# Optimization experiments

Measured on AMD Instinct MI355X. Metric: run time of the kernel, lower is better.

## Reference

```python
import jax, jax.numpy as jnp
import numpy as np

K = 16  # number of neighbors (init kwarg k)


def setup_inputs() -> dict:
    key = jax.random.key(0)
    k1, k2 = jax.random.split(key)
    B, N, D, F = 2, 2048, 16, 64
    points = jax.random.normal(k1, (B, N, D), dtype=jnp.float32)
    features = jax.random.normal(k2, (B, N, F), dtype=jnp.float32)
    return {"features": features, "points": points}


def reference(features, points):
    # points: [B, N, D]
    B, N, _ = points.shape
    # Pairwise Euclidean distances via broadcasted subtraction, matching
    # tf.norm(points[:, :, None] - points[:, None, :], axis=-1): [B, N, N]
    diff = points[:, :, None, :] - points[:, None, :, :]
    distance = jnp.sqrt(jnp.sum(diff * diff, axis=-1))
    # top (k+1) smallest distances == top_k of negated distance; drop self (col 0)
    _, topk_indices = jax.lax.top_k(-distance, K + 1)  # [B, N, K+1] int32
    topk_indices = topk_indices[:, :, 1:]               # [B, N, K]
    batch_indices = jnp.broadcast_to(
        jnp.arange(B, dtype=jnp.int32)[:, None, None, None], (B, N, K, 1)
    )
    # [B, N, K, 2] -> (batch_idx, neighbor_idx) pairs for gather_nd-style use
    return jnp.concatenate([batch_indices, topk_indices[..., None]], axis=3)
```

## Files before the change

kernel.cpp:

```cpp
#include <hip/hip_runtime.h>
#include <stdint.h>


#define NPTS 2048
#define DIMS 16
#define KK 16
#define THREADS 256
#define PER_THREAD (NPTS / THREADS)
#define HPL (THREADS / 64)

__device__ __forceinline__ void ce(uint64_t& a, uint64_t& b) {
    uint64_t lo = (a < b) ? a : b;
    uint64_t hi = (a < b) ? b : a;
    a = lo; b = hi;
}

__global__ __launch_bounds__(THREADS) void knn_kernel(
    const float* __restrict__ points, int* __restrict__ out)
{
    const int q = blockIdx.x;
    const int b = q >> 11;
    const int n = q & (NPTS - 1);
    const float* bp = points + (size_t)b * NPTS * DIMS;

    __shared__ uint64_t skeys[PER_THREAD][THREADS];
    __shared__ float    qs[DIMS];

    const int tid = threadIdx.x;
    if (tid < DIMS) qs[tid] = bp[(size_t)n * DIMS + tid];
    __syncthreads();

    float qp[DIMS];
#pragma unroll
    for (int d = 0; d < DIMS; ++d) qp[d] = qs[d];

    uint64_t k[PER_THREAD];
#pragma unroll
    for (int i = 0; i < PER_THREAD; ++i) {
        const int c = tid + i * THREADS;
        const float4* cp4 = (const float4*)(bp + (size_t)c * DIMS);
        float s[DIMS];
#pragma unroll
        for (int v = 0; v < 4; ++v) {
            float4 cv = cp4[v];
            float d0 = qp[4 * v + 0] - cv.x;
            float d1 = qp[4 * v + 1] - cv.y;
            float d2_ = qp[4 * v + 2] - cv.z;
            float d3 = qp[4 * v + 3] - cv.w;
            s[4 * v + 0] = __fmul_rn(d0, d0);
            s[4 * v + 1] = __fmul_rn(d1, d1);
            s[4 * v + 2] = __fmul_rn(d2_, d2_);
            s[4 * v + 3] = __fmul_rn(d3, d3);
        }
        float r0 = __fadd_rn(s[0], s[8]);
        float r1 = __fadd_rn(s[1], s[9]);
        float r2 = __fadd_rn(s[2], s[10]);
        float r3 = __fadd_rn(s[3], s[11]);
        float r4 = __fadd_rn(s[4], s[12]);
        float r5 = __fadd_rn(s[5], s[13]);
        float r6 = __fadd_rn(s[6], s[14]);
        float r7 = __fadd_rn(s[7], s[15]);
        float t0 = __fadd_rn(r0, r1);
        float t1 = __fadd_rn(r2, r3);
        float t2 = __fadd_rn(r4, r5);
        float t3 = __fadd_rn(r6, r7);
        float d2 = __fadd_rn(__fadd_rn(t0, t1), __fadd_rn(t2, t3));
        float dist = __fsqrt_rn(d2);
        k[i] = ((uint64_t)__float_as_uint(dist) << 32) | (uint32_t)c;
    }

    ce(k[0], k[1]); ce(k[2], k[3]); ce(k[4], k[5]); ce(k[6], k[7]);
    ce(k[0], k[2]); ce(k[1], k[3]); ce(k[4], k[6]); ce(k[5], k[7]);
    ce(k[1], k[2]); ce(k[5], k[6]);
    ce(k[0], k[4]); ce(k[1], k[5]); ce(k[2], k[6]); ce(k[3], k[7]);
    ce(k[1], k[4]); ce(k[3], k[6]);
    ce(k[2], k[4]); ce(k[3], k[5]);
    ce(k[3], k[4]);

#pragma unroll
    for (int j = 0; j < PER_THREAD; ++j) skeys[j][tid] = k[j];
    __syncthreads();

    if (tid >= 64) return;
    const int lane = tid;

    uint64_t head[HPL];
    int      pos[HPL];
#pragma unroll
    for (int h = 0; h < HPL; ++h) {
        head[h] = skeys[0][lane + 64 * h];
        pos[h] = 1;
    }

    for (int r = 0; r <= KK; ++r) {
        uint64_t m = head[0]; int hm = 0;
#pragma unroll
        for (int h = 1; h < HPL; ++h)
            if (head[h] < m) { m = head[h]; hm = h; }
        uint64_t g = m;
#pragma unroll
        for (int off = 1; off < 64; off <<= 1) {
            uint64_t o = (uint64_t)__shfl_xor((unsigned long long)g, off, 64);
            if (o < g) g = o;
        }
        if (m == g) {
            if (r > 0) {
                const int idx = (int)(uint32_t)(g & 0xffffffffu);
                const size_t o = (((size_t)q * KK) + (size_t)(r - 1)) * 2;
                out[o]     = b;
                out[o + 1] = idx;
            }
#pragma unroll
            for (int h = 0; h < HPL; ++h) {
                if (hm == h) {
                    head[h] = (pos[h] < PER_THREAD) ? skeys[pos[h]][lane + 64 * h]
                                                    : ~0ull;
                    pos[h]++;
                }
            }
        }
    }
}

extern "C" void kernel_launch(void* const* d_in, const int* in_sizes, int n_in,
                              void* d_out, int out_size, void* d_ws, size_t ws_size,
                              hipStream_t stream) {
    (void)d_ws; (void)ws_size; (void)out_size;
    const float* points;
    if (n_in >= 2 && in_sizes[1] == 2 * 2048 * 16) {
        points = (const float*)d_in[1];
    } else if (n_in >= 1 && in_sizes[0] == 2 * 2048 * 16) {
        points = (const float*)d_in[0];
    } else {
        points = (const float*)d_in[n_in - 1];
    }
    int* out = (int*)d_out;
    knn_kernel<<<2 * 2048, THREADS, 0, stream>>>(points, out);
}
```

Measured before the change: 92.35 us.

## Process four queries per block and select top-k with one wave per query

```diff
diff --git a/kernel.cpp b/kernel.cpp
--- a/kernel.cpp
+++ b/kernel.cpp
@@ -6,8 +6,11 @@
 #define DIMS 16
 #define KK 16
 #define THREADS 256
-#define PER_THREAD (NPTS / THREADS)
-#define HPL (THREADS / 64)
+#define NQ 4
+#define CPT (NPTS / THREADS)
+#define PER_LANE (NPTS / 64)
+#define RUNS 4
+#define RLEN 8
 
 __device__ __forceinline__ void ce(uint64_t& a, uint64_t& b) {
     uint64_t lo = (a < b) ? a : b;
@@ -15,88 +18,94 @@
     a = lo; b = hi;
 }
 
-__global__ __launch_bounds__(THREADS) void knn_kernel(
+__global__ __launch_bounds__(THREADS, 4) void knn_kernel(
     const float* __restrict__ points, int* __restrict__ out)
 {
-    const int q = blockIdx.x;
-    const int b = q >> 11;
-    const int n = q & (NPTS - 1);
+    const int qbase = blockIdx.x * NQ;
+    const int b = qbase >> 11;
     const float* bp = points + (size_t)b * NPTS * DIMS;
 
-    __shared__ uint64_t skeys[PER_THREAD][THREADS];
-    __shared__ float    qs[DIMS];
+    __shared__ float dist[NQ][NPTS];
 
     const int tid = threadIdx.x;
-    if (tid < DIMS) qs[tid] = bp[(size_t)n * DIMS + tid];
+
+    float qp[NQ][DIMS];
+#pragma unroll
+    for (int w = 0; w < NQ; ++w) {
+        const int n = (qbase + w) & (NPTS - 1);
+        const float4* qp4 = (const float4*)(bp + (size_t)n * DIMS);
+#pragma unroll
+        for (int v = 0; v < 4; ++v) {
+            float4 t = qp4[v];
+            qp[w][4 * v + 0] = t.x; qp[w][4 * v + 1] = t.y;
+            qp[w][4 * v + 2] = t.z; qp[w][4 * v + 3] = t.w;
+        }
+    }
+
+#pragma unroll 2
+    for (int i = 0; i < CPT; ++i) {
+        const int c = tid + i * THREADS;
+        const float4* cp4 = (const float4*)(bp + (size_t)c * DIMS);
+        float cv[DIMS];
+#pragma unroll
+        for (int v = 0; v < 4; ++v) {
+            float4 t = cp4[v];
+            cv[4 * v + 0] = t.x; cv[4 * v + 1] = t.y;
+            cv[4 * v + 2] = t.z; cv[4 * v + 3] = t.w;
+        }
+#pragma unroll
+        for (int w = 0; w < NQ; ++w) {
+            float s[DIMS];
+#pragma unroll
+            for (int d = 0; d < DIMS; ++d) {
+                float df = qp[w][d] - cv[d];
+                s[d] = __fmul_rn(df, df);
+            }
+            float r0 = __fadd_rn(s[0], s[8]);
+            float r1 = __fadd_rn(s[1], s[9]);
+            float r2 = __fadd_rn(s[2], s[10]);
+            float r3 = __fadd_rn(s[3], s[11]);
+            float r4 = __fadd_rn(s[4], s[12]);
+            float r5 = __fadd_rn(s[5], s[13]);
+            float r6 = __fadd_rn(s[6], s[14]);
+            float r7 = __fadd_rn(s[7], s[15]);
+            float t0 = __fadd_rn(r0, r1);
+            float t1 = __fadd_rn(r2, r3);
+            float t2 = __fadd_rn(r4, r5);
+            float t3 = __fadd_rn(r6, r7);
+            float d2 = __fadd_rn(__fadd_rn(t0, t1), __fadd_rn(t2, t3));
+            dist[w][c] = __fsqrt_rn(d2);
+        }
+    }
     __syncthreads();
 
-    float qp[DIMS];
+    const int w = tid >> 6;
+    const int lane = tid & 63;
+
+    uint64_t k[PER_LANE];
 #pragma unroll
-    for (int d = 0; d < DIMS; ++d) qp[d] = qs[d];
-
-    uint64_t k[PER_THREAD];
-#pragma unroll
-    for (int i = 0; i < PER_THREAD; ++i) {
-        const int c = tid + i * THREADS;
-        const float4* cp4 = (const float4*)(bp + (size_t)c * DIMS);
-        float s[DIMS];
-#pragma unroll
-        for (int v = 0; v < 4; ++v) {
-            float4 cv = cp4[v];
-            float d0 = qp[4 * v + 0] - cv.x;
-            float d1 = qp[4 * v + 1] - cv.y;
-            float d2_ = qp[4 * v + 2] - cv.z;
-            float d3 = qp[4 * v + 3] - cv.w;
-            s[4 * v + 0] = __fmul_rn(d0, d0);
-            s[4 * v + 1] = __fmul_rn(d1, d1);
-            s[4 * v + 2] = __fmul_rn(d2_, d2_);
-            s[4 * v + 3] = __fmul_rn(d3, d3);
-        }
-        float r0 = __fadd_rn(s[0], s[8]);
-        float r1 = __fadd_rn(s[1], s[9]);
-        float r2 = __fadd_rn(s[2], s[10]);
-        float r3 = __fadd_rn(s[3], s[11]);
-        float r4 = __fadd_rn(s[4], s[12]);
-        float r5 = __fadd_rn(s[5], s[13]);
-        float r6 = __fadd_rn(s[6], s[14]);
-        float r7 = __fadd_rn(s[7], s[15]);
-        float t0 = __fadd_rn(r0, r1);
-        float t1 = __fadd_rn(r2, r3);
-        float t2 = __fadd_rn(r4, r5);
-        float t3 = __fadd_rn(r6, r7);
-        float d2 = __fadd_rn(__fadd_rn(t0, t1), __fadd_rn(t2, t3));
-        float dist = __fsqrt_rn(d2);
-        k[i] = ((uint64_t)__float_as_uint(dist) << 32) | (uint32_t)c;
+    for (int j = 0; j < PER_LANE; ++j) {
+        const int c = lane + 64 * j;
+        k[j] = ((uint64_t)__float_as_uint(dist[w][c]) << 32) | (uint32_t)c;
     }
 
-    ce(k[0], k[1]); ce(k[2], k[3]); ce(k[4], k[5]); ce(k[6], k[7]);
-    ce(k[0], k[2]); ce(k[1], k[3]); ce(k[4], k[6]); ce(k[5], k[7]);
-    ce(k[1], k[2]); ce(k[5], k[6]);
-    ce(k[0], k[4]); ce(k[1], k[5]); ce(k[2], k[6]); ce(k[3], k[7]);
-    ce(k[1], k[4]); ce(k[3], k[6]);
-    ce(k[2], k[4]); ce(k[3], k[5]);
-    ce(k[3], k[4]);
-
 #pragma unroll
-    for (int j = 0; j < PER_THREAD; ++j) skeys[j][tid] = k[j];
-    __syncthreads();
-
-    if (tid >= 64) return;
-    const int lane = tid;
-
-    uint64_t head[HPL];
-    int      pos[HPL];
-#pragma unroll
-    for (int h = 0; h < HPL; ++h) {
-        head[h] = skeys[0][lane + 64 * h];
-        pos[h] = 1;
+    for (int r = 0; r < RUNS; ++r) {
+        uint64_t* p = k + r * RLEN;
+        ce(p[0], p[1]); ce(p[2], p[3]); ce(p[4], p[5]); ce(p[6], p[7]);
+        ce(p[0], p[2]); ce(p[1], p[3]); ce(p[4], p[6]); ce(p[5], p[7]);
+        ce(p[1], p[2]); ce(p[5], p[6]);
+        ce(p[0], p[4]); ce(p[1], p[5]); ce(p[2], p[6]); ce(p[3], p[7]);
+        ce(p[1], p[4]); ce(p[3], p[6]);
+        ce(p[2], p[4]); ce(p[3], p[5]);
+        ce(p[3], p[4]);
     }
 
     for (int r = 0; r <= KK; ++r) {
-        uint64_t m = head[0]; int hm = 0;
-#pragma unroll
-        for (int h = 1; h < HPL; ++h)
-            if (head[h] < m) { m = head[h]; hm = h; }
+        uint64_t m = k[0]; int hm = 0;
+        if (k[8]  < m) { m = k[8];  hm = 1; }
+        if (k[16] < m) { m = k[16]; hm = 2; }
+        if (k[24] < m) { m = k[24]; hm = 3; }
         uint64_t g = m;
 #pragma unroll
         for (int off = 1; off < 64; off <<= 1) {
@@ -105,17 +114,17 @@
         }
         if (m == g) {
             if (r > 0) {
-                const int idx = (int)(uint32_t)(g & 0xffffffffu);
-                const size_t o = (((size_t)q * KK) + (size_t)(r - 1)) * 2;
-                out[o]     = b;
-                out[o + 1] = idx;
+                int2 val;
+                val.x = b;
+                val.y = (int)(uint32_t)(g & 0xffffffffu);
+                *(int2*)(out + (((size_t)(qbase + w) * KK) + (size_t)(r - 1)) * 2) = val;
             }
 #pragma unroll
-            for (int h = 0; h < HPL; ++h) {
+            for (int h = 0; h < RUNS; ++h) {
                 if (hm == h) {
-                    head[h] = (pos[h] < PER_THREAD) ? skeys[pos[h]][lane + 64 * h]
-                                                    : ~0ull;
-                    pos[h]++;
+#pragma unroll
+                    for (int j = 0; j < RLEN - 1; ++j) k[h * RLEN + j] = k[h * RLEN + j + 1];
+                    k[h * RLEN + RLEN - 1] = ~0ull;
                 }
             }
         }
@@ -135,5 +144,5 @@
         points = (const float*)d_in[n_in - 1];
     }
     int* out = (int*)d_out;
-    knn_kernel<<<2 * 2048, THREADS, 0, stream>>>(points, out);
+    knn_kernel<<<(2 * 2048) / NQ, THREADS, 0, stream>>>(points, out);
 }
```

Measured after the change: 86.99 us. 1.06x faster.
